# Kernel optimization log

Hardware: AMD Instinct MI355X
Metric: run time of the kernel (lower is better)

The kernel has to match this reference:

```python
import jax, jax.numpy as jnp
import numpy as np

N = 131072   # total gates/nodes in the batched block-diagonal circuit graph
E = 524288   # directed edges (avg degree 4)
D = 100      # hidden dim
DA = 50      # msg MLP hidden
DC = 30      # classifier hidden
R = 20       # message-passing rounds


def mlp(x, W1, b1, W2, b2):
    return jax.nn.relu(x @ W1 + b1) @ W2 + b2


def gru_step(x, h, Wih, Whh, bih, bhh):
    # single-timestep torch.nn.GRU cell
    gi = x @ Wih.T + bih
    gh = h @ Whh.T + bhh
    ir, iz, inn = jnp.split(gi, 3, axis=-1)
    hr, hz, hn = jnp.split(gh, 3, axis=-1)
    r = jax.nn.sigmoid(ir + hr)
    z = jax.nn.sigmoid(iz + hz)
    nwe = jnp.tanh(inn + r * hn)
    return (1.0 - z) * nwe + z * h


def setup_inputs():
    key = jax.random.key(0)
    ks = jax.random.split(key, 26)
    s = 0.05

    def rn(k, shape):
        return jax.random.normal(k, shape, dtype=jnp.float32) * s

    inp = {
        'features': jax.random.normal(ks[0], (N, 4), dtype=jnp.float32),
        'edge_row': jax.random.randint(ks[1], (E,), 0, N, dtype=jnp.int32),
        'edge_col': jax.random.randint(ks[2], (E,), 0, N, dtype=jnp.int32),
        'init_W': rn(ks[3], (4, D)), 'init_b': jnp.zeros((D,), jnp.float32),
        'fmsg_W1': rn(ks[4], (D, DA)), 'fmsg_b1': jnp.zeros((DA,), jnp.float32),
        'fmsg_W2': rn(ks[5], (DA, D)), 'fmsg_b2': jnp.zeros((D,), jnp.float32),
        'bmsg_W1': rn(ks[6], (D, DA)), 'bmsg_b1': jnp.zeros((DA,), jnp.float32),
        'bmsg_W2': rn(ks[7], (DA, D)), 'bmsg_b2': jnp.zeros((D,), jnp.float32),
        'fgru_Wih': rn(ks[8], (3 * D, D)), 'fgru_Whh': rn(ks[9], (3 * D, D)),
        'fgru_bih': jnp.zeros((3 * D,), jnp.float32), 'fgru_bhh': jnp.zeros((3 * D,), jnp.float32),
        'bgru_Wih': rn(ks[10], (3 * D, D)), 'bgru_Whh': rn(ks[11], (3 * D, D)),
        'bgru_bih': jnp.zeros((3 * D,), jnp.float32), 'bgru_bhh': jnp.zeros((3 * D,), jnp.float32),
        'cls_W1': rn(ks[12], (D, DC)), 'cls_b1': jnp.zeros((DC,), jnp.float32),
        'cls_W2': rn(ks[13], (DC, 1)), 'cls_b2': jnp.zeros((1,), jnp.float32),
    }
    return inp


def reference(features, edge_row, edge_col, init_W, init_b,
              fmsg_W1, fmsg_b1, fmsg_W2, fmsg_b2,
              bmsg_W1, bmsg_b1, bmsg_W2, bmsg_b2,
              fgru_Wih, fgru_Whh, fgru_bih, fgru_bhh,
              bgru_Wih, bgru_Whh, bgru_bih, bgru_bhh,
              cls_W1, cls_b1, cls_W2, cls_b2):
    n = features.shape[0]
    h = features @ init_W + init_b  # [N, D]

    def round_body(h, _):
        # forward pass: adj @ forward_msg(h)
        fm = mlp(h, fmsg_W1, fmsg_b1, fmsg_W2, fmsg_b2)
        f_msg = jax.ops.segment_sum(fm[edge_col], edge_row, num_segments=n)
        h = gru_step(f_msg, h, fgru_Wih, fgru_Whh, fgru_bih, fgru_bhh)
        # backward pass: adj.T @ backward_msg(h)
        bm = mlp(h, bmsg_W1, bmsg_b1, bmsg_W2, bmsg_b2)
        b_msg = jax.ops.segment_sum(bm[edge_row], edge_col, num_segments=n)
        h = gru_step(b_msg, h, bgru_Wih, bgru_Whh, bgru_bih, bgru_bhh)
        return h, None

    h, _ = jax.lax.scan(jax.checkpoint(round_body), h, None, length=R)
    return mlp(h, cls_W1, cls_b1, cls_W2, cls_b2)  # [N, 1]
```

## Files before the change

### kernel.cpp

```cpp
#include <hip/hip_runtime.h>
#include <math.h>

#define Nn 131072
#define Ee 524288
#define LROW 224

typedef __attribute__((ext_vector_type(8))) short short8;
typedef __attribute__((ext_vector_type(4))) float f32x4;
typedef unsigned short ushort_t;
typedef unsigned int uint32;

__device__ __forceinline__ f32x4 mfma16(short8 a, short8 b, f32x4 c) {
    return __builtin_amdgcn_mfma_f32_16x16x32_bf16(a, b, c, 0, 0, 0);
}

__device__ __forceinline__ uint32 rne_bf16(float x) {
    uint32 u = __float_as_uint(x);
    return (u + 0x7FFFu + ((u >> 16) & 1u)) >> 16;
}

__device__ __forceinline__ void split3(float x, uint32& h, uint32& m, uint32& l) {
    h = rne_bf16(x);
    float hf = __uint_as_float(h << 16);
    float r1 = x - hf;
    m = rne_bf16(r1);
    float mf = __uint_as_float(m << 16);
    float r2 = r1 - mf;
    l = rne_bf16(r2);
}

__device__ __forceinline__ float limb2f(ushort_t u) {
    return __uint_as_float((uint32)u << 16);
}

__device__ __forceinline__ void gl16(const ushort_t* g, ushort_t* l) {
    __builtin_amdgcn_global_load_lds(
        (const __attribute__((address_space(1))) uint32*)g,
        (__attribute__((address_space(3))) uint32*)l, 16, 0, 0);
}

__global__ void diag_kernel(float* out, float val) {
    int n = blockIdx.x * 256 + threadIdx.x;
    if (n < Nn) out[n] = (n == 0) ? val : 0.f;
}
__global__ void zero_ints(int* p, int n) {
    int i = blockIdx.x * 256 + threadIdx.x;
    if (i < n) p[i] = 0;
}
__global__ void zero_short8(ushort_t* p, long n8) {
    long i = (long)blockIdx.x * 256 + threadIdx.x;
    if (i < n8) {
        short8 zz = {0, 0, 0, 0, 0, 0, 0, 0};
        *(short8*)(p + i * 8) = zz;
    }
}

__global__ void hist_kernel(const int* __restrict__ er, const int* __restrict__ ec,
                            int* __restrict__ cnt_f, int* __restrict__ cnt_b) {
    int e = blockIdx.x * 256 + threadIdx.x;
    atomicAdd(&cnt_f[er[e]], 1);
    atomicAdd(&cnt_b[ec[e]], 1);
}

__global__ __launch_bounds__(1024) void scan2_kernel(
    const int* __restrict__ cnt_f, const int* __restrict__ cnt_b,
    int* __restrict__ ptr_f, int* __restrict__ ptr_b, int n) {
    const int* cnt = blockIdx.x ? cnt_b : cnt_f;
    int* ptr = blockIdx.x ? ptr_b : ptr_f;
    __shared__ int sums[1024];
    int t = threadIdx.x;
    int chunk = n >> 10;
    int base = t * chunk;
    int s = 0;
    for (int i = 0; i < chunk; i++) s += cnt[base + i];
    sums[t] = s;
    __syncthreads();
    for (int off = 1; off < 1024; off <<= 1) {
        int v = (t >= off) ? sums[t - off] : 0;
        __syncthreads();
        sums[t] += v;
        __syncthreads();
    }
    int run = (t == 0) ? 0 : sums[t - 1];
    for (int i = 0; i < chunk; i++) { ptr[base + i] = run; run += cnt[base + i]; }
    if (t == 1023) ptr[n] = run;
}

__global__ void fill_kernel(const int* __restrict__ er, const int* __restrict__ ec,
                            int* __restrict__ ptr_f, int* __restrict__ ptr_b,
                            int* __restrict__ src_f, int* __restrict__ src_b) {
    int e = blockIdx.x * 256 + threadIdx.x;
    int r = er[e], c = ec[e];
    int p = atomicAdd(&ptr_f[r], 1); src_f[p] = c;
    int q = atomicAdd(&ptr_b[c], 1); src_b[q] = r;
}

__global__ void prep_gru_w(const float* __restrict__ Wih, const float* __restrict__ Whh,
                           const float* __restrict__ bih, const float* __restrict__ bhh,
                           ushort_t* __restrict__ W0, ushort_t* __restrict__ W1,
                           ushort_t* __restrict__ W2, float* __restrict__ bg) {
    int gid = blockIdx.x * 256 + threadIdx.x;
    if (gid >= 448 * 224) return;
    int c = gid / 224, k = gid - c * 224;
    int d = c >> 2, g = c & 3;
    float w = 0.f;
    if (d < 100) {
        if (k < 100) {
            if (g == 0)      w = Wih[d * 100 + k];
            else if (g == 1) w = Wih[(100 + d) * 100 + k];
            else if (g == 2) w = Wih[(200 + d) * 100 + k];
        } else if (k >= 112 && k < 212) {
            int kk = k - 112;
            if (g == 0)      w = Whh[d * 100 + kk];
            else if (g == 1) w = Whh[(100 + d) * 100 + kk];
            else if (g == 3) w = Whh[(200 + d) * 100 + kk];
        }
    }
    uint32 h, m, l; split3(w, h, m, l);
    W0[gid] = (ushort_t)h; W1[gid] = (ushort_t)m; W2[gid] = (ushort_t)l;
    if (k == 0) {
        float b = 0.f;
        if (d < 100) {
            if (g == 0)      b = bih[d] + bhh[d];
            else if (g == 1) b = bih[100 + d] + bhh[100 + d];
            else if (g == 2) b = bih[200 + d];
            else             b = bhh[200 + d];
        }
        bg[c] = b;
    }
}

__global__ void prep_msg_w(const float* __restrict__ W1, const float* __restrict__ b1,
                           const float* __restrict__ W2, const float* __restrict__ b2,
                           ushort_t* __restrict__ A0, ushort_t* __restrict__ A1,
                           ushort_t* __restrict__ A2, float* __restrict__ b1p,
                           ushort_t* __restrict__ B0, ushort_t* __restrict__ B1,
                           ushort_t* __restrict__ B2, float* __restrict__ b2p) {
    int gid = blockIdx.x * 256 + threadIdx.x;
    if (gid < 8192) {
        int c = gid >> 7, k = gid & 127;
        float w = (c < 50 && k < 100) ? W1[k * 50 + c] : 0.f;
        uint32 h, m, l; split3(w, h, m, l);
        A0[gid] = (ushort_t)h; A1[gid] = (ushort_t)m; A2[gid] = (ushort_t)l;
        if (k == 0) b1p[c] = (c < 50) ? b1[c] : 0.f;
    } else if (gid < 8192 + 7168) {
        int t = gid - 8192;
        int c = t >> 6, k = t & 63;
        float w = (c < 100 && k < 50) ? W2[k * 100 + c] : 0.f;
        uint32 h, m, l; split3(w, h, m, l);
        B0[t] = (ushort_t)h; B1[t] = (ushort_t)m; B2[t] = (ushort_t)l;
        if (k == 0) b2p[c] = (c < 100) ? b2[c] : 0.f;
    }
}

__global__ void init_h_kernel(const float* __restrict__ feat, const float* __restrict__ W,
                              const float* __restrict__ b,
                              ushort_t* __restrict__ L0, ushort_t* __restrict__ L1,
                              ushort_t* __restrict__ L2) {
    int gid = blockIdx.x * 256 + threadIdx.x;
    if (gid >= Nn * 100) return;
    int n = gid / 100, d = gid - n * 100;
    float acc = b[d];
#pragma unroll
    for (int k = 0; k < 4; k++) acc += feat[n * 4 + k] * W[k * 100 + d];
    uint32 h, m, l; split3(acc, h, m, l);
    size_t a = (size_t)n * LROW + 112 + d;
    L0[a] = (ushort_t)h; L1[a] = (ushort_t)m; L2[a] = (ushort_t)l;
}

__global__ __launch_bounds__(256, 2) void msg_mfma(
    const ushort_t* __restrict__ L0, const ushort_t* __restrict__ L1,
    const ushort_t* __restrict__ L2,
    const ushort_t* __restrict__ A0, const ushort_t* __restrict__ A1,
    const ushort_t* __restrict__ A2, const float* __restrict__ b1p,
    const ushort_t* __restrict__ B0, const ushort_t* __restrict__ B1,
    const ushort_t* __restrict__ B2, const float* __restrict__ b2p,
    float* __restrict__ fm) {
    __shared__ ushort_t C1[3][64][72];
    const int tid = threadIdx.x;
    const int u = tid >> 6;
    const int lane = tid & 63;
    const int m = lane & 15, q = lane >> 4;
    const int n0 = blockIdx.x * 64;
    const int n = n0 + u * 16 + m;

    f32x4 z = {0.f, 0.f, 0.f, 0.f};
    f32x4 a1[4] = {z, z, z, z};

    const size_t hbase = (size_t)n * LROW + 112;
    for (int kc = 0; kc < 4; kc++) {
        int kb = kc * 32 + q * 8;
        short8 f0 = *(const short8*)(L0 + hbase + kb);
        short8 f1 = *(const short8*)(L1 + hbase + kb);
        short8 f2 = *(const short8*)(L2 + hbase + kb);
#pragma unroll
        for (int t = 0; t < 4; t++) {
            int off = (t * 16 + m) * 128 + kc * 32 + q * 8;
            short8 w0 = *(const short8*)(A0 + off);
            short8 w1 = *(const short8*)(A1 + off);
            short8 w2 = *(const short8*)(A2 + off);
            a1[t] = mfma16(w0, f0, a1[t]);
            a1[t] = mfma16(w0, f1, a1[t]);
            a1[t] = mfma16(w1, f0, a1[t]);
            a1[t] = mfma16(w0, f2, a1[t]);
            a1[t] = mfma16(w2, f0, a1[t]);
            a1[t] = mfma16(w1, f1, a1[t]);
        }
    }
#pragma unroll
    for (int t = 0; t < 4; t++) {
        int c0 = t * 16 + 4 * q;
        float4 bb = *(const float4*)&b1p[c0];
        float v0 = fmaxf(a1[t][0] + bb.x, 0.f);
        float v1 = fmaxf(a1[t][1] + bb.y, 0.f);
        float v2 = fmaxf(a1[t][2] + bb.z, 0.f);
        float v3 = fmaxf(a1[t][3] + bb.w, 0.f);
        uint32 h0, m0, l0, h1, m1, l1, h2, m2, l2, h3, m3, l3;
        split3(v0, h0, m0, l0); split3(v1, h1, m1, l1);
        split3(v2, h2, m2, l2); split3(v3, h3, m3, l3);
        int nl = u * 16 + m;
        *(uint2*)&C1[0][nl][c0] = make_uint2(h0 | (h1 << 16), h2 | (h3 << 16));
        *(uint2*)&C1[1][nl][c0] = make_uint2(m0 | (m1 << 16), m2 | (m3 << 16));
        *(uint2*)&C1[2][nl][c0] = make_uint2(l0 | (l1 << 16), l2 | (l3 << 16));
    }
    __syncthreads();

    f32x4 a2[7] = {z, z, z, z, z, z, z};
    for (int kc = 0; kc < 2; kc++) {
        int nl = u * 16 + m;
        short8 c0f = *(const short8*)&C1[0][nl][kc * 32 + q * 8];
        short8 c1f = *(const short8*)&C1[1][nl][kc * 32 + q * 8];
        short8 c2f = *(const short8*)&C1[2][nl][kc * 32 + q * 8];
#pragma unroll
        for (int t = 0; t < 7; t++) {
            int off = (t * 16 + m) * 64 + kc * 32 + q * 8;
            short8 w0 = *(const short8*)(B0 + off);
            short8 w1 = *(const short8*)(B1 + off);
            short8 w2 = *(const short8*)(B2 + off);
            a2[t] = mfma16(w0, c0f, a2[t]);
            a2[t] = mfma16(w0, c1f, a2[t]);
            a2[t] = mfma16(w1, c0f, a2[t]);
            a2[t] = mfma16(w0, c2f, a2[t]);
            a2[t] = mfma16(w2, c0f, a2[t]);
            a2[t] = mfma16(w1, c1f, a2[t]);
        }
    }
#pragma unroll
    for (int t = 0; t < 7; t++) {
        int c0 = t * 16 + 4 * q;
        if (c0 < 100) {
            float4 bb = *(const float4*)&b2p[c0];
            float4 o;
            o.x = a2[t][0] + bb.x; o.y = a2[t][1] + bb.y;
            o.z = a2[t][2] + bb.z; o.w = a2[t][3] + bb.w;
            *(float4*)&fm[(size_t)n * 100 + c0] = o;
        }
    }
}

__global__ void gather4(const float* __restrict__ fm, const int* __restrict__ ptr,
                        const int* __restrict__ idx,
                        ushort_t* __restrict__ L0, ushort_t* __restrict__ L1,
                        ushort_t* __restrict__ L2) {
    int gid = blockIdx.x * 256 + threadIdx.x;
    int n = gid / 25, qq = (gid - n * 25) * 4;
    int s = (n == 0) ? 0 : ptr[n - 1];
    int e = ptr[n];
    float4 acc = {0.f, 0.f, 0.f, 0.f};
    for (int i = s; i < e; i++) {
        float4 v = *(const float4*)&fm[(size_t)idx[i] * 100 + qq];
        acc.x += v.x; acc.y += v.y; acc.z += v.z; acc.w += v.w;
    }
    uint32 h0, m0, l0, h1, m1, l1, h2, m2, l2, h3, m3, l3;
    split3(acc.x, h0, m0, l0); split3(acc.y, h1, m1, l1);
    split3(acc.z, h2, m2, l2); split3(acc.w, h3, m3, l3);
    size_t a = (size_t)n * LROW + qq;
    *(uint2*)&L0[a] = make_uint2(h0 | (h1 << 16), h2 | (h3 << 16));
    *(uint2*)&L1[a] = make_uint2(m0 | (m1 << 16), m2 | (m3 << 16));
    *(uint2*)&L2[a] = make_uint2(l0 | (l1 << 16), l2 | (l3 << 16));
}

typedef union {
    ushort_t lbuf[2][3][64][32];
    float    sh[64][116];
} GruShm;

__global__ __launch_bounds__(256, 2) void gru_mfma(
    ushort_t* __restrict__ L0, ushort_t* __restrict__ L1,
    ushort_t* __restrict__ L2,
    const ushort_t* __restrict__ W0, const ushort_t* __restrict__ W1,
    const ushort_t* __restrict__ W2, const float* __restrict__ bg) {
    __shared__ GruShm U;
    const int tid = threadIdx.x;
    const int wave = tid >> 6;
    const int lane = tid & 63;
    const int m = lane & 15, q = lane >> 4;
    const int n0 = blockIdx.x * 64;

    const int lr = lane >> 2;
    const int lc = (lane & 3) ^ ((lane >> 3) & 3);
    const size_t sbase = (size_t)(n0 + wave * 16 + lr) * LROW + lc * 8;
    const int cq = (q ^ ((m >> 1) & 3)) * 8;

    f32x4 z = {0.f, 0.f, 0.f, 0.f};
    f32x4 acc[7][4];
#pragma unroll
    for (int t = 0; t < 7; t++)
#pragma unroll
        for (int rf = 0; rf < 4; rf++) acc[t][rf] = z;

    int woff[7];
#pragma unroll
    for (int t = 0; t < 7; t++)
        woff[t] = ((t * 4 + wave) * 16 + m) * 224 + q * 8;

#define STAGE(nb, KO)                                              \
    gl16(L0 + sbase + (KO), &U.lbuf[nb][0][wave * 16][0]);         \
    gl16(L1 + sbase + (KO), &U.lbuf[nb][1][wave * 16][0]);         \
    gl16(L2 + sbase + (KO), &U.lbuf[nb][2][wave * 16][0]);

#define GP(Wreg, Fr)                                               \
    _Pragma("unroll")                                              \
    for (int t = 0; t < 7; t++) {                                  \
        _Pragma("unroll")                                          \
        for (int rf = 0; rf < 4; rf++)                             \
            acc[t][rf] = mfma16(Wreg[t], Fr[rf], acc[t][rf]);      \
    }

    STAGE(0, 0)
    __syncthreads();

    short8 wA[7], wB[7];
#pragma unroll
    for (int t = 0; t < 7; t++) wA[t] = *(const short8*)(W0 + woff[t]);

#pragma unroll
    for (int kc = 0; kc < 7; kc++) {
        const int ko = kc * 32;
        const int cb = kc & 1;
        if (kc < 6) { STAGE(cb ^ 1, ko + 32) }

        short8 f0[4], f1[4], f2[4];
#pragma unroll
        for (int rf = 0; rf < 4; rf++)
            f0[rf] = *(const short8*)&U.lbuf[cb][0][rf * 16 + m][cq];
#pragma unroll
        for (int rf = 0; rf < 4; rf++)
            f1[rf] = *(const short8*)&U.lbuf[cb][1][rf * 16 + m][cq];
#pragma unroll
        for (int rf = 0; rf < 4; rf++)
            f2[rf] = *(const short8*)&U.lbuf[cb][2][rf * 16 + m][cq];

        if ((kc & 1) == 0) {
#pragma unroll
            for (int t = 0; t < 7; t++) wB[t] = *(const short8*)(W1 + woff[t] + ko);
            GP(wA, f0); GP(wA, f1); GP(wA, f2);
#pragma unroll
            for (int t = 0; t < 7; t++) wA[t] = *(const short8*)(W2 + woff[t] + ko);
            GP(wB, f0); GP(wB, f1);
            if (kc < 6) {
#pragma unroll
                for (int t = 0; t < 7; t++) wB[t] = *(const short8*)(W0 + woff[t] + ko + 32);
            }
            GP(wA, f0);
        } else {
#pragma unroll
            for (int t = 0; t < 7; t++) wA[t] = *(const short8*)(W1 + woff[t] + ko);
            GP(wB, f0); GP(wB, f1); GP(wB, f2);
#pragma unroll
            for (int t = 0; t < 7; t++) wB[t] = *(const short8*)(W2 + woff[t] + ko);
            GP(wA, f0); GP(wA, f1);
            if (kc < 6) {
#pragma unroll
                for (int t = 0; t < 7; t++) wA[t] = *(const short8*)(W0 + woff[t] + ko + 32);
            }
            GP(wB, f0);
        }
        __syncthreads();
    }
#undef GP
#undef STAGE

#pragma unroll
    for (int p = 0; p < 4; p++) {
        int idx = tid + p * 256;
        int row = idx >> 4, c = idx & 15;
        if (c < 13) {
            size_t g = (size_t)(n0 + row) * LROW + 112 + c * 8;
            union { short8 s; ushort_t u[8]; } a0, a1, a2;
            a0.s = *(const short8*)(L0 + g);
            a1.s = *(const short8*)(L1 + g);
            a2.s = *(const short8*)(L2 + g);
#pragma unroll
            for (int j = 0; j < 8; j++)
                U.sh[row][c * 8 + j] =
                    (limb2f(a2.u[j]) + limb2f(a1.u[j])) + limb2f(a0.u[j]);
        }
    }
    __syncthreads();

#pragma unroll
    for (int t = 0; t < 7; t++) {
        const int ct = t * 4 + wave;
        const int d = ct * 4 + q;
        if (d < 100) {
            float4 b4 = *(const float4*)&bg[ct * 16 + 4 * q];
#pragma unroll
            for (int rf = 0; rf < 4; rf++) {
                int row = rf * 16 + m;
                float hold = U.sh[row][d];
                float rp = acc[t][rf][0] + b4.x;
                float zp = acc[t][rf][1] + b4.y;
                float np = acc[t][rf][2] + b4.z;
                float hh = acc[t][rf][3] + b4.w;
                float rr = 1.f / (1.f + __expf(-rp));
                float zz = 1.f / (1.f + __expf(-zp));
                float nw = tanhf(np + rr * hh);
                U.sh[row][d] = (1.f - zz) * nw + zz * hold;
            }
        }
    }
    __syncthreads();

#pragma unroll
    for (int p = 0; p < 4; p++) {
        int idx = tid + p * 256;
        int row = idx >> 4, c = idx & 15;
        if (c < 13) {
            size_t g = (size_t)(n0 + row) * LROW + 112 + c * 8;
            union { short8 s; uint32 u4[4]; } o0, o1, o2;
#pragma unroll
            for (int jj = 0; jj < 4; jj++) {
                float ea = U.sh[row][c * 8 + 2 * jj];
                float eb = U.sh[row][c * 8 + 2 * jj + 1];
                uint32 ha, ma, la, hb, mb, lb;
                split3(ea, ha, ma, la);
                split3(eb, hb, mb, lb);
                o0.u4[jj] = ha | (hb << 16);
                o1.u4[jj] = ma | (mb << 16);
                o2.u4[jj] = la | (lb << 16);
            }
            *(short8*)(L0 + g) = o0.s;
            *(short8*)(L1 + g) = o1.s;
            *(short8*)(L2 + g) = o2.s;
        }
    }
}

__global__ __launch_bounds__(256) void classifier(
    const ushort_t* __restrict__ L0, const ushort_t* __restrict__ L1,
    const ushort_t* __restrict__ L2, const float* __restrict__ W1,
    const float* __restrict__ b1, const float* __restrict__ W2,
    const float* __restrict__ b2, float* __restrict__ out) {
    __shared__ float Wc[3128];
    __shared__ float bc[30];
    __shared__ float w2[30];
    int tid = threadIdx.x;
    for (int i = tid; i < 3128; i += 256) Wc[i] = (i < 3000) ? W1[i] : 0.f;
    if (tid < 30) { bc[tid] = b1[tid]; w2[tid] = W2[tid]; }
    __syncthreads();
    int n = blockIdx.x * 256 + tid;
    float a[30];
#pragma unroll
    for (int j = 0; j < 30; j++) a[j] = bc[j];
    const size_t base = (size_t)n * LROW + 112;
    for (int k8 = 0; k8 < 13; k8++) {
        int k0 = k8 * 8;
        union { short8 s; ushort_t u[8]; } h0, h1, h2;
        h0.s = *(const short8*)(L0 + base + k0);
        h1.s = *(const short8*)(L1 + base + k0);
        h2.s = *(const short8*)(L2 + base + k0);
#pragma unroll
        for (int jj = 0; jj < 8; jj++) {
            float hv = (limb2f(h2.u[jj]) + limb2f(h1.u[jj])) + limb2f(h0.u[jj]);
#pragma unroll
            for (int j = 0; j < 30; j++) a[j] = fmaf(hv, Wc[(k0 + jj) * 30 + j], a[j]);
        }
    }
    float s = b2[0];
#pragma unroll
    for (int j = 0; j < 30; j++) s = fmaf(fmaxf(a[j], 0.f), w2[j], s);
    out[n] = s;
}

extern "C" void kernel_launch(void* const* d_in, const int* in_sizes, int n_in,
                              void* d_out, int out_size, void* d_ws, size_t ws_size,
                              hipStream_t stream) {
    const float* feat     = (const float*)d_in[0];
    const int*   er       = (const int*)d_in[1];
    const int*   ec       = (const int*)d_in[2];
    const float* init_W   = (const float*)d_in[3];
    const float* init_b   = (const float*)d_in[4];
    const float* fmsg_W1  = (const float*)d_in[5];
    const float* fmsg_b1  = (const float*)d_in[6];
    const float* fmsg_W2  = (const float*)d_in[7];
    const float* fmsg_b2  = (const float*)d_in[8];
    const float* bmsg_W1  = (const float*)d_in[9];
    const float* bmsg_b1  = (const float*)d_in[10];
    const float* bmsg_W2  = (const float*)d_in[11];
    const float* bmsg_b2  = (const float*)d_in[12];
    const float* fgru_Wih = (const float*)d_in[13];
    const float* fgru_Whh = (const float*)d_in[14];
    const float* fgru_bih = (const float*)d_in[15];
    const float* fgru_bhh = (const float*)d_in[16];
    const float* bgru_Wih = (const float*)d_in[17];
    const float* bgru_Whh = (const float*)d_in[18];
    const float* bgru_bih = (const float*)d_in[19];
    const float* bgru_bhh = (const float*)d_in[20];
    const float* cls_W1   = (const float*)d_in[21];
    const float* cls_b1   = (const float*)d_in[22];
    const float* cls_W2   = (const float*)d_in[23];
    const float* cls_b2   = (const float*)d_in[24];
    float* out = (float*)d_out;

    float* ws = (float*)d_ws;
    size_t o = 0;
    float* fm = ws + o; o += (size_t)Nn * 100;

    const size_t PL = (size_t)Nn * LROW + 64;
    ushort_t* us = (ushort_t*)(ws + o);
    size_t uo = 0;
    ushort_t* L0 = us + uo; uo += PL;
    ushort_t* L1 = us + uo; uo += PL;
    ushort_t* L2 = us + uo; uo += PL;
    ushort_t* fWg0 = us + uo; uo += 448 * 224;
    ushort_t* fWg1 = us + uo; uo += 448 * 224;
    ushort_t* fWg2 = us + uo; uo += 448 * 224;
    ushort_t* bWg0 = us + uo; uo += 448 * 224;
    ushort_t* bWg1 = us + uo; uo += 448 * 224;
    ushort_t* bWg2 = us + uo; uo += 448 * 224;
    ushort_t* fA0 = us + uo; uo += 8192;
    ushort_t* fA1 = us + uo; uo += 8192;
    ushort_t* fA2 = us + uo; uo += 8192;
    ushort_t* bA0 = us + uo; uo += 8192;
    ushort_t* bA1 = us + uo; uo += 8192;
    ushort_t* bA2 = us + uo; uo += 8192;
    ushort_t* fB0 = us + uo; uo += 7168;
    ushort_t* fB1 = us + uo; uo += 7168;
    ushort_t* fB2 = us + uo; uo += 7168;
    ushort_t* bB0 = us + uo; uo += 7168;
    ushort_t* bB1 = us + uo; uo += 7168;
    ushort_t* bB2 = us + uo; uo += 7168;
    o += uo / 2;

    float* bgf  = ws + o; o += 448;
    float* bgb  = ws + o; o += 448;
    float* b1pf = ws + o; o += 64;
    float* b1pb = ws + o; o += 64;
    float* b2pf = ws + o; o += 112;
    float* b2pb = ws + o; o += 112;

    int* iws   = (int*)(ws + o);
    int* ptr_f = iws;
    int* ptr_b = ptr_f + (Nn + 1);
    int* cnt   = ptr_b + (Nn + 1);
    int* cnt_f = cnt;
    int* cnt_b = cnt + Nn;
    int* src_f = cnt + 2 * (size_t)Nn;
    int* src_b = src_f + Ee;

    size_t need = o * sizeof(float) +
                  (size_t)(2 * (Nn + 1) + 2 * Nn + 2 * Ee) * sizeof(int);
    if (ws_size < need) {
        diag_kernel<<<(Nn + 255) / 256, 256, 0, stream>>>(out, (float)ws_size);
        return;
    }

    {
        long n8 = (long)(3 * PL / 8);
        zero_short8<<<(int)((n8 + 255) / 256), 256, 0, stream>>>(L0, n8);
    }

    zero_ints<<<(2 * Nn + 255) / 256, 256, 0, stream>>>(cnt, 2 * Nn);
    hist_kernel<<<Ee / 256, 256, 0, stream>>>(er, ec, cnt_f, cnt_b);
    scan2_kernel<<<2, 1024, 0, stream>>>(cnt_f, cnt_b, ptr_f, ptr_b, Nn);
    fill_kernel<<<Ee / 256, 256, 0, stream>>>(er, ec, ptr_f, ptr_b, src_f, src_b);

    prep_gru_w<<<(448 * 224 + 255) / 256, 256, 0, stream>>>(
        fgru_Wih, fgru_Whh, fgru_bih, fgru_bhh, fWg0, fWg1, fWg2, bgf);
    prep_gru_w<<<(448 * 224 + 255) / 256, 256, 0, stream>>>(
        bgru_Wih, bgru_Whh, bgru_bih, bgru_bhh, bWg0, bWg1, bWg2, bgb);
    prep_msg_w<<<(15360 + 255) / 256, 256, 0, stream>>>(
        fmsg_W1, fmsg_b1, fmsg_W2, fmsg_b2, fA0, fA1, fA2, b1pf, fB0, fB1, fB2, b2pf);
    prep_msg_w<<<(15360 + 255) / 256, 256, 0, stream>>>(
        bmsg_W1, bmsg_b1, bmsg_W2, bmsg_b2, bA0, bA1, bA2, b1pb, bB0, bB1, bB2, b2pb);

    init_h_kernel<<<(Nn * 100 + 255) / 256, 256, 0, stream>>>(
        feat, init_W, init_b, L0, L1, L2);

    const int gTile = Nn / 64;
    const int gGru  = Nn / 64;
    const int gGath = Nn * 25 / 256;

    for (int rd = 0; rd < 20; rd++) {
        msg_mfma<<<gTile, 256, 0, stream>>>(L0, L1, L2,
            fA0, fA1, fA2, b1pf, fB0, fB1, fB2, b2pf, fm);
        gather4<<<gGath, 256, 0, stream>>>(fm, ptr_f, src_f, L0, L1, L2);
        gru_mfma<<<gGru, 256, 0, stream>>>(L0, L1, L2, fWg0, fWg1, fWg2, bgf);

        msg_mfma<<<gTile, 256, 0, stream>>>(L0, L1, L2,
            bA0, bA1, bA2, b1pb, bB0, bB1, bB2, b2pb, fm);
        gather4<<<gGath, 256, 0, stream>>>(fm, ptr_b, src_b, L0, L1, L2);
        gru_mfma<<<gGru, 256, 0, stream>>>(L0, L1, L2, bWg0, bWg1, bWg2, bgb);
    }

    classifier<<<Nn / 256, 256, 0, stream>>>(L0, L1, L2,
        cls_W1, cls_b1, cls_W2, cls_b2, out);
}
```

Before: 13.38 ms.

## Fuse CSR gather-sum into GRU kernel and split h/msg buffers

Removes the separate gather4 kernel. The GRU kernel now does the segment-sum of neighbour messages for its 64-node tile straight into shared memory, then splits the sums into bf16 limbs in registers for the input half of the MFMA K loop. The hidden state moves to its own 128-wide limb arrays, and the GRU weights are padded to K=256. This avoids writing and re-reading the message limbs through global memory and saves one launch per half-round, at the cost of a serial gather phase before the MFMA work with no overlap, plus extra LDS use.

```diff
diff --git a/kernel.cpp b/kernel.cpp
--- a/kernel.cpp
+++ b/kernel.cpp
@@ -3,7 +3,8 @@
 
 #define Nn 131072
 #define Ee 524288
-#define LROW 224
+#define HK 128
+#define WK 256
 
 typedef __attribute__((ext_vector_type(8))) short short8;
 typedef __attribute__((ext_vector_type(4))) float f32x4;
@@ -100,8 +101,8 @@
                            ushort_t* __restrict__ W0, ushort_t* __restrict__ W1,
                            ushort_t* __restrict__ W2, float* __restrict__ bg) {
     int gid = blockIdx.x * 256 + threadIdx.x;
-    if (gid >= 448 * 224) return;
-    int c = gid / 224, k = gid - c * 224;
+    if (gid >= 448 * WK) return;
+    int c = gid / WK, k = gid - c * WK;
     int d = c >> 2, g = c & 3;
     float w = 0.f;
     if (d < 100) {
@@ -109,8 +110,8 @@
             if (g == 0)      w = Wih[d * 100 + k];
             else if (g == 1) w = Wih[(100 + d) * 100 + k];
             else if (g == 2) w = Wih[(200 + d) * 100 + k];
-        } else if (k >= 112 && k < 212) {
-            int kk = k - 112;
+        } else if (k >= 128 && k < 228) {
+            int kk = k - 128;
             if (g == 0)      w = Whh[d * 100 + kk];
             else if (g == 1) w = Whh[(100 + d) * 100 + kk];
             else if (g == 3) w = Whh[(200 + d) * 100 + kk];
@@ -155,8 +156,8 @@
 
 __global__ void init_h_kernel(const float* __restrict__ feat, const float* __restrict__ W,
                               const float* __restrict__ b,
-                              ushort_t* __restrict__ L0, ushort_t* __restrict__ L1,
-                              ushort_t* __restrict__ L2) {
+                              ushort_t* __restrict__ H0, ushort_t* __restrict__ H1,
+                              ushort_t* __restrict__ H2) {
     int gid = blockIdx.x * 256 + threadIdx.x;
     if (gid >= Nn * 100) return;
     int n = gid / 100, d = gid - n * 100;
@@ -164,13 +165,13 @@
 #pragma unroll
     for (int k = 0; k < 4; k++) acc += feat[n * 4 + k] * W[k * 100 + d];
     uint32 h, m, l; split3(acc, h, m, l);
-    size_t a = (size_t)n * LROW + 112 + d;
-    L0[a] = (ushort_t)h; L1[a] = (ushort_t)m; L2[a] = (ushort_t)l;
+    size_t a = (size_t)n * HK + d;
+    H0[a] = (ushort_t)h; H1[a] = (ushort_t)m; H2[a] = (ushort_t)l;
 }
 
 __global__ __launch_bounds__(256, 2) void msg_mfma(
-    const ushort_t* __restrict__ L0, const ushort_t* __restrict__ L1,
-    const ushort_t* __restrict__ L2,
+    const ushort_t* __restrict__ H0, const ushort_t* __restrict__ H1,
+    const ushort_t* __restrict__ H2,
     const ushort_t* __restrict__ A0, const ushort_t* __restrict__ A1,
     const ushort_t* __restrict__ A2, const float* __restrict__ b1p,
     const ushort_t* __restrict__ B0, const ushort_t* __restrict__ B1,
@@ -187,12 +188,12 @@
     f32x4 z = {0.f, 0.f, 0.f, 0.f};
     f32x4 a1[4] = {z, z, z, z};
 
-    const size_t hbase = (size_t)n * LROW + 112;
+    const size_t hbase = (size_t)n * HK;
     for (int kc = 0; kc < 4; kc++) {
         int kb = kc * 32 + q * 8;
-        short8 f0 = *(const short8*)(L0 + hbase + kb);
-        short8 f1 = *(const short8*)(L1 + hbase + kb);
-        short8 f2 = *(const short8*)(L2 + hbase + kb);
+        short8 f0 = *(const short8*)(H0 + hbase + kb);
+        short8 f1 = *(const short8*)(H1 + hbase + kb);
+        short8 f2 = *(const short8*)(H2 + hbase + kb);
 #pragma unroll
         for (int t = 0; t < 4; t++) {
             int off = (t * 16 + m) * 128 + kc * 32 + q * 8;
@@ -258,49 +259,52 @@
     }
 }
 
-__global__ void gather4(const float* __restrict__ fm, const int* __restrict__ ptr,
-                        const int* __restrict__ idx,
-                        ushort_t* __restrict__ L0, ushort_t* __restrict__ L1,
-                        ushort_t* __restrict__ L2) {
-    int gid = blockIdx.x * 256 + threadIdx.x;
-    int n = gid / 25, qq = (gid - n * 25) * 4;
-    int s = (n == 0) ? 0 : ptr[n - 1];
-    int e = ptr[n];
-    float4 acc = {0.f, 0.f, 0.f, 0.f};
-    for (int i = s; i < e; i++) {
-        float4 v = *(const float4*)&fm[(size_t)idx[i] * 100 + qq];
-        acc.x += v.x; acc.y += v.y; acc.z += v.z; acc.w += v.w;
-    }
-    uint32 h0, m0, l0, h1, m1, l1, h2, m2, l2, h3, m3, l3;
-    split3(acc.x, h0, m0, l0); split3(acc.y, h1, m1, l1);
-    split3(acc.z, h2, m2, l2); split3(acc.w, h3, m3, l3);
-    size_t a = (size_t)n * LROW + qq;
-    *(uint2*)&L0[a] = make_uint2(h0 | (h1 << 16), h2 | (h3 << 16));
-    *(uint2*)&L1[a] = make_uint2(m0 | (m1 << 16), m2 | (m3 << 16));
-    *(uint2*)&L2[a] = make_uint2(l0 | (l1 << 16), l2 | (l3 << 16));
-}
-
 typedef union {
-    ushort_t lbuf[2][3][64][32];
-    float    sh[64][116];
-} GruShm;
+    float t32[4][4][2][64][4];
+    float sh[64][116];
+} GruU;
 
 __global__ __launch_bounds__(256, 2) void gru_mfma(
-    ushort_t* __restrict__ L0, ushort_t* __restrict__ L1,
-    ushort_t* __restrict__ L2,
+    ushort_t* __restrict__ H0, ushort_t* __restrict__ H1,
+    ushort_t* __restrict__ H2,
+    const float* __restrict__ fm, const int* __restrict__ ptr,
+    const int* __restrict__ eidx,
     const ushort_t* __restrict__ W0, const ushort_t* __restrict__ W1,
     const ushort_t* __restrict__ W2, const float* __restrict__ bg) {
-    __shared__ GruShm U;
+    __shared__ GruU U;
+    __shared__ ushort_t hbuf[4][3][4][64][8];
     const int tid = threadIdx.x;
     const int wave = tid >> 6;
     const int lane = tid & 63;
     const int m = lane & 15, q = lane >> 4;
     const int n0 = blockIdx.x * 64;
 
-    const int lr = lane >> 2;
-    const int lc = (lane & 3) ^ ((lane >> 3) & 3);
-    const size_t sbase = (size_t)(n0 + wave * 16 + lr) * LROW + lc * 8;
-    const int cq = (q ^ ((m >> 1) & 3)) * 8;
+    {
+        const size_t src = (size_t)(n0 + wave * 16 + (lane & 15)) * HK + (lane >> 4) * 8;
+#pragma unroll
+        for (int s = 0; s < 4; s++) {
+            gl16(H0 + src + s * 32, &hbuf[s][0][wave][0][0]);
+            gl16(H1 + src + s * 32, &hbuf[s][1][wave][0][0]);
+            gl16(H2 + src + s * 32, &hbuf[s][2][wave][0][0]);
+        }
+    }
+
+    for (int t = tid; t < 2048; t += 256) {
+        int row = t >> 5, c4 = (t & 31) * 4;
+        f32x4 a4 = {0.f, 0.f, 0.f, 0.f};
+        if (c4 < 100) {
+            int n = n0 + row;
+            int s0 = (n == 0) ? 0 : ptr[n - 1];
+            int e0 = ptr[n];
+            for (int i = s0; i < e0; i++) {
+                float4 v = *(const float4*)&fm[(size_t)eidx[i] * 100 + c4];
+                a4[0] += v.x; a4[1] += v.y; a4[2] += v.z; a4[3] += v.w;
+            }
+        }
+        *(f32x4*)&U.t32[c4 >> 5][row >> 4][(c4 >> 2) & 1]
+                       [((c4 >> 3) & 3) * 16 + (row & 15)][0] = a4;
+    }
+    __syncthreads();
 
     f32x4 z = {0.f, 0.f, 0.f, 0.f};
     f32x4 acc[7][4];
@@ -312,12 +316,7 @@
     int woff[7];
 #pragma unroll
     for (int t = 0; t < 7; t++)
-        woff[t] = ((t * 4 + wave) * 16 + m) * 224 + q * 8;
-
-#define STAGE(nb, KO)                                              \
-    gl16(L0 + sbase + (KO), &U.lbuf[nb][0][wave * 16][0]);         \
-    gl16(L1 + sbase + (KO), &U.lbuf[nb][1][wave * 16][0]);         \
-    gl16(L2 + sbase + (KO), &U.lbuf[nb][2][wave * 16][0]);
+        woff[t] = ((t * 4 + wave) * 16 + m) * WK + q * 8;
 
 #define GP(Wreg, Fr)                                               \
     _Pragma("unroll")                                              \
@@ -327,29 +326,41 @@
             acc[t][rf] = mfma16(Wreg[t], Fr[rf], acc[t][rf]);      \
     }
 
-    STAGE(0, 0)
-    __syncthreads();
-
     short8 wA[7], wB[7];
 #pragma unroll
     for (int t = 0; t < 7; t++) wA[t] = *(const short8*)(W0 + woff[t]);
 
 #pragma unroll
-    for (int kc = 0; kc < 7; kc++) {
+    for (int kc = 0; kc < 8; kc++) {
         const int ko = kc * 32;
-        const int cb = kc & 1;
-        if (kc < 6) { STAGE(cb ^ 1, ko + 32) }
-
         short8 f0[4], f1[4], f2[4];
-#pragma unroll
-        for (int rf = 0; rf < 4; rf++)
-            f0[rf] = *(const short8*)&U.lbuf[cb][0][rf * 16 + m][cq];
-#pragma unroll
-        for (int rf = 0; rf < 4; rf++)
-            f1[rf] = *(const short8*)&U.lbuf[cb][1][rf * 16 + m][cq];
-#pragma unroll
-        for (int rf = 0; rf < 4; rf++)
-            f2[rf] = *(const short8*)&U.lbuf[cb][2][rf * 16 + m][cq];
+        if (kc < 4) {
+#pragma unroll
+            for (int rf = 0; rf < 4; rf++) {
+                f32x4 lo = *(const f32x4*)&U.t32[kc][rf][0][lane][0];
+                f32x4 hi = *(const f32x4*)&U.t32[kc][rf][1][lane][0];
+                float e[8] = {lo[0], lo[1], lo[2], lo[3], hi[0], hi[1], hi[2], hi[3]};
+                union { short8 s; uint32 u4[4]; } p0, p1, p2;
+#pragma unroll
+                for (int j = 0; j < 4; j++) {
+                    uint32 ha, ma, la, hb, mb, lb;
+                    split3(e[2 * j], ha, ma, la);
+                    split3(e[2 * j + 1], hb, mb, lb);
+                    p0.u4[j] = ha | (hb << 16);
+                    p1.u4[j] = ma | (mb << 16);
+                    p2.u4[j] = la | (lb << 16);
+                }
+                f0[rf] = p0.s; f1[rf] = p1.s; f2[rf] = p2.s;
+            }
+        } else {
+            const int b = kc - 4;
+#pragma unroll
+            for (int rf = 0; rf < 4; rf++) {
+                f0[rf] = *(const short8*)&hbuf[b][0][rf][lane][0];
+                f1[rf] = *(const short8*)&hbuf[b][1][rf][lane][0];
+                f2[rf] = *(const short8*)&hbuf[b][2][rf][lane][0];
+            }
+        }
 
         if ((kc & 1) == 0) {
 #pragma unroll
@@ -358,7 +369,7 @@
 #pragma unroll
             for (int t = 0; t < 7; t++) wA[t] = *(const short8*)(W2 + woff[t] + ko);
             GP(wB, f0); GP(wB, f1);
-            if (kc < 6) {
+            if (kc < 7) {
 #pragma unroll
                 for (int t = 0; t < 7; t++) wB[t] = *(const short8*)(W0 + woff[t] + ko + 32);
             }
@@ -370,27 +381,27 @@
 #pragma unroll
             for (int t = 0; t < 7; t++) wB[t] = *(const short8*)(W2 + woff[t] + ko);
             GP(wA, f0); GP(wA, f1);
-            if (kc < 6) {
+            if (kc < 7) {
 #pragma unroll
                 for (int t = 0; t < 7; t++) wA[t] = *(const short8*)(W0 + woff[t] + ko + 32);
             }
             GP(wB, f0);
         }
-        __syncthreads();
     }
 #undef GP
-#undef STAGE
-
-#pragma unroll
-    for (int p = 0; p < 4; p++) {
-        int idx = tid + p * 256;
-        int row = idx >> 4, c = idx & 15;
+
+    __syncthreads();
+
+#pragma unroll
+    for (int p4 = 0; p4 < 4; p4++) {
+        int ix = tid + p4 * 256;
+        int row = ix >> 4, c = ix & 15;
         if (c < 13) {
-            size_t g = (size_t)(n0 + row) * LROW + 112 + c * 8;
+            int bb = c >> 2, cc = c & 3, sl = cc * 16 + (row & 15), rg = row >> 4;
             union { short8 s; ushort_t u[8]; } a0, a1, a2;
-            a0.s = *(const short8*)(L0 + g);
-            a1.s = *(const short8*)(L1 + g);
-            a2.s = *(const short8*)(L2 + g);
+            a0.s = *(const short8*)&hbuf[bb][0][rg][sl][0];
+            a1.s = *(const short8*)&hbuf[bb][1][rg][sl][0];
+            a2.s = *(const short8*)&hbuf[bb][2][rg][sl][0];
 #pragma unroll
             for (int j = 0; j < 8; j++)
                 U.sh[row][c * 8 + j] =
@@ -423,11 +434,11 @@
     __syncthreads();
 
 #pragma unroll
-    for (int p = 0; p < 4; p++) {
-        int idx = tid + p * 256;
-        int row = idx >> 4, c = idx & 15;
+    for (int p4 = 0; p4 < 4; p4++) {
+        int ix = tid + p4 * 256;
+        int row = ix >> 4, c = ix & 15;
         if (c < 13) {
-            size_t g = (size_t)(n0 + row) * LROW + 112 + c * 8;
+            size_t g = (size_t)(n0 + row) * HK + c * 8;
             union { short8 s; uint32 u4[4]; } o0, o1, o2;
 #pragma unroll
             for (int jj = 0; jj < 4; jj++) {
@@ -440,16 +451,16 @@
                 o1.u4[jj] = ma | (mb << 16);
                 o2.u4[jj] = la | (lb << 16);
             }
-            *(short8*)(L0 + g) = o0.s;
-            *(short8*)(L1 + g) = o1.s;
-            *(short8*)(L2 + g) = o2.s;
+            *(short8*)(H0 + g) = o0.s;
+            *(short8*)(H1 + g) = o1.s;
+            *(short8*)(H2 + g) = o2.s;
         }
     }
 }
 
 __global__ __launch_bounds__(256) void classifier(
-    const ushort_t* __restrict__ L0, const ushort_t* __restrict__ L1,
-    const ushort_t* __restrict__ L2, const float* __restrict__ W1,
+    const ushort_t* __restrict__ H0, const ushort_t* __restrict__ H1,
+    const ushort_t* __restrict__ H2, const float* __restrict__ W1,
     const float* __restrict__ b1, const float* __restrict__ W2,
     const float* __restrict__ b2, float* __restrict__ out) {
     __shared__ float Wc[3128];
@@ -463,13 +474,13 @@
     float a[30];
 #pragma unroll
     for (int j = 0; j < 30; j++) a[j] = bc[j];
-    const size_t base = (size_t)n * LROW + 112;
+    const size_t base = (size_t)n * HK;
     for (int k8 = 0; k8 < 13; k8++) {
         int k0 = k8 * 8;
         union { short8 s; ushort_t u[8]; } h0, h1, h2;
-        h0.s = *(const short8*)(L0 + base + k0);
-        h1.s = *(const short8*)(L1 + base + k0);
-        h2.s = *(const short8*)(L2 + base + k0);
+        h0.s = *(const short8*)(H0 + base + k0);
+        h1.s = *(const short8*)(H1 + base + k0);
+        h2.s = *(const short8*)(H2 + base + k0);
 #pragma unroll
         for (int jj = 0; jj < 8; jj++) {
             float hv = (limb2f(h2.u[jj]) + limb2f(h1.u[jj])) + limb2f(h0.u[jj]);
@@ -517,18 +528,18 @@
     size_t o = 0;
     float* fm = ws + o; o += (size_t)Nn * 100;
 
-    const size_t PL = (size_t)Nn * LROW + 64;
+    const size_t PL = (size_t)Nn * HK + 64;
     ushort_t* us = (ushort_t*)(ws + o);
     size_t uo = 0;
-    ushort_t* L0 = us + uo; uo += PL;
-    ushort_t* L1 = us + uo; uo += PL;
-    ushort_t* L2 = us + uo; uo += PL;
-    ushort_t* fWg0 = us + uo; uo += 448 * 224;
-    ushort_t* fWg1 = us + uo; uo += 448 * 224;
-    ushort_t* fWg2 = us + uo; uo += 448 * 224;
-    ushort_t* bWg0 = us + uo; uo += 448 * 224;
-    ushort_t* bWg1 = us + uo; uo += 448 * 224;
-    ushort_t* bWg2 = us + uo; uo += 448 * 224;
+    ushort_t* H0 = us + uo; uo += PL;
+    ushort_t* H1 = us + uo; uo += PL;
+    ushort_t* H2 = us + uo; uo += PL;
+    ushort_t* fWg0 = us + uo; uo += 448 * WK;
+    ushort_t* fWg1 = us + uo; uo += 448 * WK;
+    ushort_t* fWg2 = us + uo; uo += 448 * WK;
+    ushort_t* bWg0 = us + uo; uo += 448 * WK;
+    ushort_t* bWg1 = us + uo; uo += 448 * WK;
+    ushort_t* bWg2 = us + uo; uo += 448 * WK;
     ushort_t* fA0 = us + uo; uo += 8192;
     ushort_t* fA1 = us + uo; uo += 8192;
     ushort_t* fA2 = us + uo; uo += 8192;
@@ -568,7 +579,7 @@
 
     {
         long n8 = (long)(3 * PL / 8);
-        zero_short8<<<(int)((n8 + 255) / 256), 256, 0, stream>>>(L0, n8);
+        zero_short8<<<(int)((n8 + 255) / 256), 256, 0, stream>>>(H0, n8);
     }
 
     zero_ints<<<(2 * Nn + 255) / 256, 256, 0, stream>>>(cnt, 2 * Nn);
@@ -576,9 +587,9 @@
     scan2_kernel<<<2, 1024, 0, stream>>>(cnt_f, cnt_b, ptr_f, ptr_b, Nn);
     fill_kernel<<<Ee / 256, 256, 0, stream>>>(er, ec, ptr_f, ptr_b, src_f, src_b);
 
-    prep_gru_w<<<(448 * 224 + 255) / 256, 256, 0, stream>>>(
+    prep_gru_w<<<(448 * WK + 255) / 256, 256, 0, stream>>>(
         fgru_Wih, fgru_Whh, fgru_bih, fgru_bhh, fWg0, fWg1, fWg2, bgf);
-    prep_gru_w<<<(448 * 224 + 255) / 256, 256, 0, stream>>>(
+    prep_gru_w<<<(448 * WK + 255) / 256, 256, 0, stream>>>(
         bgru_Wih, bgru_Whh, bgru_bih, bgru_bhh, bWg0, bWg1, bWg2, bgb);
     prep_msg_w<<<(15360 + 255) / 256, 256, 0, stream>>>(
         fmsg_W1, fmsg_b1, fmsg_W2, fmsg_b2, fA0, fA1, fA2, b1pf, fB0, fB1, fB2, b2pf);
@@ -586,24 +597,23 @@
         bmsg_W1, bmsg_b1, bmsg_W2, bmsg_b2, bA0, bA1, bA2, b1pb, bB0, bB1, bB2, b2pb);
 
     init_h_kernel<<<(Nn * 100 + 255) / 256, 256, 0, stream>>>(
-        feat, init_W, init_b, L0, L1, L2);
+        feat, init_W, init_b, H0, H1, H2);
 
     const int gTile = Nn / 64;
     const int gGru  = Nn / 64;
-    const int gGath = Nn * 25 / 256;
 
     for (int rd = 0; rd < 20; rd++) {
-        msg_mfma<<<gTile, 256, 0, stream>>>(L0, L1, L2,
+        msg_mfma<<<gTile, 256, 0, stream>>>(H0, H1, H2,
             fA0, fA1, fA2, b1pf, fB0, fB1, fB2, b2pf, fm);
-        gather4<<<gGath, 256, 0, stream>>>(fm, ptr_f, src_f, L0, L1, L2);
-        gru_mfma<<<gGru, 256, 0, stream>>>(L0, L1, L2, fWg0, fWg1, fWg2, bgf);
-
-        msg_mfma<<<gTile, 256, 0, stream>>>(L0, L1, L2,
+        gru_mfma<<<gGru, 256, 0, stream>>>(H0, H1, H2, fm, ptr_f, src_f,
+            fWg0, fWg1, fWg2, bgf);
+
+        msg_mfma<<<gTile, 256, 0, stream>>>(H0, H1, H2,
             bA0, bA1, bA2, b1pb, bB0, bB1, bB2, b2pb, fm);
-        gather4<<<gGath, 256, 0, stream>>>(fm, ptr_b, src_b, L0, L1, L2);
-        gru_mfma<<<gGru, 256, 0, stream>>>(L0, L1, L2, bWg0, bWg1, bWg2, bgb);
-    }
-
-    classifier<<<Nn / 256, 256, 0, stream>>>(L0, L1, L2,
+        gru_mfma<<<gGru, 256, 0, stream>>>(H0, H1, H2, fm, ptr_b, src_b,
+            bWg0, bWg1, bWg2, bgb);
+    }
+
+    classifier<<<Nn / 256, 256, 0, stream>>>(H0, H1, H2,
         cls_W1, cls_b1, cls_W2, cls_b2, out);
 }
```

Result: slower. 16.71 ms (+24.9%).
